# Performance work log

Measured on AMD Instinct MI355X. Metric: run time of the kernel, lower is better.

## Reference

```python
import jax, jax.numpy as jnp
import numpy as np

TAU = 0.2          # rank_temperature
LAM = 8.0          # lambda_value
TOPO = 0.5         # topology_influence
LEN_C = 0.01       # edge_length_coeff
SP_C = 0.001       # edge_sparsity_coeff
B, M, D = 4096, 256, 256


def _pairwise_sq(a, b):
    # [Na, D] x [Nb, D] -> [Na, Nb] squared L2 distances
    sq = (jnp.sum(a * a, -1)[:, None] - 2.0 * (a @ b.T)
          + jnp.sum(b * b, -1)[None, :])
    return jnp.maximum(sq, 0.0)


def setup_inputs() -> dict:
    key = jax.random.key(0)
    k1, k2, k3 = jax.random.split(key, 3)
    data = jax.random.normal(k1, (B, D), dtype=jnp.float32)
    weights = jax.random.uniform(k2, (M, D), dtype=jnp.float32)
    # edge logits initialized near edge_init_logit (-2.0) with small noise
    edge_logits = -2.0 + 0.1 * jax.random.normal(k3, (M, M), dtype=jnp.float32)
    return {"data": data, "weights": weights, "edge_logits": edge_logits}


def reference(data, weights, edge_logits):
    m = weights.shape[0]
    eye = jnp.eye(m, dtype=data.dtype)

    # distances: [B, M], l2
    distances = jnp.sqrt(_pairwise_sq(data, weights))

    # soft rank: [B, M]; pairwise sigmoid with zeroed diagonal
    diff = (distances[:, :, None] - distances[:, None, :]) / TAU  # [B, M, M]
    prob_greater = jax.nn.sigmoid(diff) * (1.0 - eye)[None]
    soft_rank = 1.0 + jnp.sum(prob_greater, axis=-1)

    # exponential neighborhood weighting
    neighborhood = jnp.exp(-(soft_rank - 1.0) / LAM)

    # symmetric edge probabilities with zero diagonal
    logits = 0.5 * (edge_logits + edge_logits.T)
    edge_prob = jax.nn.sigmoid(logits) * (1.0 - eye)

    degree = jnp.sum(edge_prob, axis=1) / float(m - 1)
    neighborhood = neighborhood * (1.0 + TOPO * degree[None, :])

    data_term = jnp.mean(neighborhood * distances)

    proto_dist = _pairwise_sq(weights, weights)  # sq_l2
    weighted_len = jnp.sum(edge_prob * proto_dist) / (jnp.sum(edge_prob) + 1e-8)
    sparsity = jnp.mean(edge_prob)

    loss = data_term + LEN_C * weighted_len + SP_C * sparsity
    return loss
```

## Files before the change

### kernel.cpp

```cpp
#include <hip/hip_runtime.h>
#include <math.h>

#define B_N 4096
#define M_N 256
#define D_N 256
#define ROWS 4
#define GRID_MAIN (B_N / ROWS)
#define NSLOT 64
#define BLK_PER_SLOT (GRID_MAIN / NSLOT)

constexpr float TAU_   = 0.2f;
constexpr float LAM_   = 8.0f;
constexpr float TOPO_  = 0.5f;
constexpr float LEN_C_ = 0.01f;
constexpr float SP_C_  = 0.001f;
constexpr float LOG2E_ = 1.44269504088896340736f;
constexpr float KSC    = LOG2E_ / TAU_;
constexpr float KL     = LOG2E_ / LAM_;
constexpr float C0_    = 133.0f;


__device__ __forceinline__ float wave_reduce_sum(float v) {
#pragma unroll
  for (int off = 1; off < 64; off <<= 1) v += __shfl_xor(v, off, 64);
  return v;
}

__device__ __forceinline__ void rank_quad(float iv, float iv2, float4 q,
                                          float& s) {
  float ta = fmaf(q.x, iv, 1.0f);
  float da = fmaf(q.y, iv2, ta);
  float na = ta + 1.0f;
  float tb = fmaf(q.z, iv, 1.0f);
  float db = fmaf(q.w, iv2, tb);
  float nb = tb + 1.0f;
  float d4 = da * db;
  float n4 = fmaf(na, db, nb * da);
  s = fmaf(n4, __builtin_amdgcn_rcpf(d4), s);
}

__global__ __launch_bounds__(256) void k_prep(const float* __restrict__ w,
                                              const float* __restrict__ E,
                                              float* __restrict__ ws) {
  int tid = threadIdx.x;
  if (blockIdx.x < M_N) {
    float* wT = ws + 8192;
    int j = blockIdx.x, d = tid;
    float v = w[j * D_N + d];
    wT[d * M_N + j] = v;
    float s = wave_reduce_sum(v * v);
    __shared__ float red[4];
    if ((d & 63) == 0) red[d >> 6] = s;
    if (j == 0) {
      if (d < 16) ws[d] = 0.0f;
      if (d < NSLOT) {
        ws[2048 + 16 * d] = 0.0f;
        ((unsigned*)ws)[4096 + 16 * d] = 0u;
      }
    }
    __syncthreads();
    if (d == 0) ws[512 + j] = red[0] + red[1] + red[2] + red[3];
  } else {
    int j = blockIdx.x - M_N;
    int k = tid;
    __shared__ __align__(16) float sp[M_N];
    __shared__ float redp[4], redt[4];

    float l = 0.5f * (E[j * M_N + k] + E[k * M_N + j]);
    float p = __builtin_amdgcn_rcpf(1.0f + __builtin_amdgcn_exp2f(-l * LOG2E_));
    if (k == j) p = 0.0f;
    sp[k] = p;

    float spw = wave_reduce_sum(p);
    if ((k & 63) == 0) redp[k >> 6] = spw;
    __syncthreads();
    float tp = redp[0] + redp[1] + redp[2] + redp[3];

    float A = 0.0f, Bv = 0.0f;
    const float4* sp4 = (const float4*)sp;
    const float* wb = w + tid;
#pragma unroll 4
    for (int k0 = 0; k0 < M_N / 4; k0++) {
      float4 pq = sp4[k0];
      const float* wr = wb + (size_t)(4 * k0) * D_N;
      float w0 = wr[0], w1 = wr[D_N], w2 = wr[2 * D_N], w3 = wr[3 * D_N];
      A  = fmaf(pq.x, w0 * w0, A); Bv = fmaf(pq.x, w0, Bv);
      A  = fmaf(pq.y, w1 * w1, A); Bv = fmaf(pq.y, w1, Bv);
      A  = fmaf(pq.z, w2 * w2, A); Bv = fmaf(pq.z, w2, Bv);
      A  = fmaf(pq.w, w3 * w3, A); Bv = fmaf(pq.w, w3, Bv);
    }

    float wj = w[j * D_N + tid];
    float v  = fmaf(tp, wj * wj, fmaf(-2.0f * wj, Bv, A));
    float sv = wave_reduce_sum(v);
    if ((k & 63) == 0) redt[k >> 6] = sv;
    __syncthreads();
    if (k == 0) {
      float tw = redt[0] + redt[1] + redt[2] + redt[3];
      ws[16 + j]   = tp * (1.0f / (float)(M_N - 1));
      ws[1024 + j] = tp;
      ws[1280 + j] = tw;
    }
  }
}

__global__ __launch_bounds__(256, 4) void k_main(const float* __restrict__ data,
                                                 float* __restrict__ ws,
                                                 float* __restrict__ out) {
  const float* wT     = ws + 8192;
  const float* wnorm  = ws + 512;
  const float* degree = ws + 16;
  float* S_slot  = ws + 2048;
  unsigned* cnt1 = (unsigned*)ws + 4096;
  unsigned* cnt2 = (unsigned*)ws + 4;

  __shared__ __align__(16) float ew[ROWS][M_N];
  __shared__ __align__(16) float ewp[ROWS][M_N];
  __shared__ float rednrm[ROWS][4];
  __shared__ float snrm[ROWS];
  __shared__ float redf[4], redp[4], redw[4];
  __shared__ int isLast;

  const int tid  = threadIdx.x;
  const int wv_  = tid >> 6;
  const int lane = tid & 63;
  const int b0   = blockIdx.x * ROWS;

#pragma unroll
  for (int r = 0; r < ROWS; r++) {
    float x = data[(size_t)(b0 + r) * D_N + tid];
    float s = wave_reduce_sum(x * x);
    if (lane == 0) rednrm[r][wv_] = s;
  }
  __syncthreads();
  if (tid < ROWS)
    snrm[tid] = rednrm[tid][0] + rednrm[tid][1] + rednrm[tid][2] + rednrm[tid][3];

  const float4* x0 = (const float4*)(data + (size_t)(b0 + 0) * D_N);
  const float4* x1 = (const float4*)(data + (size_t)(b0 + 1) * D_N);
  const float4* x2 = (const float4*)(data + (size_t)(b0 + 2) * D_N);
  const float4* x3 = (const float4*)(data + (size_t)(b0 + 3) * D_N);
  const float* pw = wT + tid;

  float a0 = 0.f, a1 = 0.f, a2 = 0.f, a3 = 0.f;
  float wreg[2][16];
#pragma unroll
  for (int i = 0; i < 16; i++) wreg[0][i] = pw[(size_t)i * M_N];

#pragma unroll
  for (int g = 0; g < 16; g++) {
    const int cur = g & 1, nxt = cur ^ 1;
    if (g < 15) {
#pragma unroll
      for (int i = 0; i < 16; i++)
        wreg[nxt][i] = pw[(size_t)((g + 1) * 16 + i) * M_N];
    }
#pragma unroll
    for (int i4 = 0; i4 < 4; i4++) {
      int d4 = 4 * g + i4;
      float4 xa = x0[d4], xb = x1[d4], xc = x2[d4], xd = x3[d4];
      float w0 = wreg[cur][4 * i4 + 0], w1 = wreg[cur][4 * i4 + 1];
      float w2 = wreg[cur][4 * i4 + 2], w3 = wreg[cur][4 * i4 + 3];
      a0 = fmaf(xa.x, w0, a0); a0 = fmaf(xa.y, w1, a0);
      a0 = fmaf(xa.z, w2, a0); a0 = fmaf(xa.w, w3, a0);
      a1 = fmaf(xb.x, w0, a1); a1 = fmaf(xb.y, w1, a1);
      a1 = fmaf(xb.z, w2, a1); a1 = fmaf(xb.w, w3, a1);
      a2 = fmaf(xc.x, w0, a2); a2 = fmaf(xc.y, w1, a2);
      a2 = fmaf(xc.z, w2, a2); a2 = fmaf(xc.w, w3, a2);
      a3 = fmaf(xd.x, w0, a3); a3 = fmaf(xd.y, w1, a3);
      a3 = fmaf(xd.z, w2, a3); a3 = fmaf(xd.w, w3, a3);
    }
  }
  __syncthreads();

  float wn = wnorm[tid];
  float acc[ROWS] = {a0, a1, a2, a3};
  float dist[ROWS], iv[ROWS], iv2[ROWS];
#pragma unroll
  for (int r = 0; r < ROWS; r++) {
    float sq = snrm[r] - 2.0f * acc[r] + wn;
    dist[r] = sqrtf(fmaxf(sq, 0.0f));
    float sc = dist[r] * KSC;
    ew[r][tid] = __builtin_amdgcn_exp2f(sc - C0_);
    iv[r]      = __builtin_amdgcn_exp2f(C0_ - sc);
    iv2[r]     = iv[r] * iv[r];
  }
  __syncthreads();

#pragma unroll
  for (int h = 0; h < 2; h++) {
    int p  = tid + h * 256;
    int r  = p >> 7, idx = p & 127;
    float ea = ew[r][2 * idx], eb = ew[r][2 * idx + 1];
    ewp[r][2 * idx]     = ea + eb;
    ewp[r][2 * idx + 1] = ea * eb;
  }
  __syncthreads();

  float fj = 1.0f + TOPO_ * degree[tid];
  float tl = 0.0f;
#pragma unroll
  for (int r = 0; r < ROWS; r++) {
    float s = 0.0f;
    const float4* q4 = (const float4*)(&ewp[r][0]);
    float ivr = iv[r], iv2r = iv2[r];
#pragma unroll 8
    for (int k4 = 0; k4 < M_N / 4; k4++) {
      float4 q = q4[k4];
      rank_quad(ivr, iv2r, q, s);
    }
    float nb = __builtin_amdgcn_exp2f((0.5f - s) * KL);
    tl = fmaf(nb * dist[r], fj, tl);
  }

  float bs = wave_reduce_sum(tl);
  if (lane == 0) redf[wv_] = bs;
  __syncthreads();
  if (tid == 0) {
    float tot = redf[0] + redf[1] + redf[2] + redf[3];
    int slot = (int)(blockIdx.x & (NSLOT - 1));
    float old = atomicAdd(&S_slot[16 * slot], tot);
    asm volatile("" : "+v"(old));
    int last = 0;
    unsigned t1 = atomicAdd(&cnt1[16 * slot], 1u);
    if (t1 == (unsigned)(BLK_PER_SLOT - 1)) {
      unsigned t2 = atomicAdd(cnt2, 1u);
      last = (t2 == (unsigned)(NSLOT - 1)) ? 1 : 0;
    }
    isLast = last;
  }
  __syncthreads();

  if (isLast) {
    float p  = ws[1024 + tid];
    float wd = ws[1280 + tid];
    float rp = wave_reduce_sum(p);
    float rw = wave_reduce_sum(wd);
    if (lane == 0) { redp[wv_] = rp; redw[wv_] = rw; }
    float sd = 0.0f;
    if (wv_ == 0) {
      float v = atomicAdd(&S_slot[16 * lane], 0.0f);
      sd = wave_reduce_sum(v);
    }
    __syncthreads();
    if (tid == 0) {
      float Sp   = redp[0] + redp[1] + redp[2] + redp[3];
      float Swpd = redw[0] + redw[1] + redw[2] + redw[3];
      float data_term = sd * (1.0f / ((float)B_N * (float)M_N));
      float wl = Swpd / (Sp + 1e-8f);
      float sparsity = Sp * (1.0f / ((float)M_N * (float)M_N));
      out[0] = data_term + LEN_C_ * wl + SP_C_ * sparsity;
    }
  }
}

extern "C" void kernel_launch(void* const* d_in, const int* in_sizes, int n_in,
                              void* d_out, int out_size, void* d_ws, size_t ws_size,
                              hipStream_t stream) {
  const float* data = (const float*)d_in[0];
  const float* w    = (const float*)d_in[1];
  const float* E    = (const float*)d_in[2];
  float* ws = (float*)d_ws;

  k_prep<<<2 * M_N, 256, 0, stream>>>(w, E, ws);
  k_main<<<GRID_MAIN, 256, 0, stream>>>(data, ws, (float*)d_out);
}
```

Baseline: 100.9 us.

## Compute data-prototype dot products with split-bf16 MFMA instead of scalar FMA

Replaces the per-thread FP32 FMA loop for the data·weights dot products with bf16 MFMA 16x16x32 instructions. Both operands are split into high and low bf16 parts and three products are accumulated to approximate FP32 accuracy. The prep kernel now stores the weights as row-major bf16 hi/lo arrays, and k_main stages the data rows as bf16 hi/lo in shared memory and writes the results through a new shared dotq buffer. With only 4 rows per block, most of each 16-row MFMA tile is wasted, since rows repeat across columns. The split-bf16 scheme also drops the lo*lo term, which adds a small precision loss.

```diff
diff --git a/kernel.cpp b/kernel.cpp
--- a/kernel.cpp
+++ b/kernel.cpp
@@ -20,10 +20,22 @@
 constexpr float C0_    = 133.0f;
 
 
+typedef __attribute__((ext_vector_type(8))) short bf16x8;
+typedef __attribute__((ext_vector_type(4))) float f32x4;
+
 __device__ __forceinline__ float wave_reduce_sum(float v) {
 #pragma unroll
   for (int off = 1; off < 64; off <<= 1) v += __shfl_xor(v, off, 64);
   return v;
+}
+
+__device__ __forceinline__ unsigned short f2bf(float f) {
+  unsigned u = __float_as_uint(f);
+  unsigned r = (u + 0x7FFFu + ((u >> 16) & 1u)) >> 16;
+  return (unsigned short)r;
+}
+__device__ __forceinline__ float bf2f(unsigned short h) {
+  return __uint_as_float(((unsigned)h) << 16);
 }
 
 __device__ __forceinline__ void rank_quad(float iv, float iv2, float4 q,
@@ -44,10 +56,15 @@
                                               float* __restrict__ ws) {
   int tid = threadIdx.x;
   if (blockIdx.x < M_N) {
-    float* wT = ws + 8192;
+    unsigned short* wbh = (unsigned short*)(ws + 8192);
+    unsigned short* wbl = (unsigned short*)(ws + 40960);
     int j = blockIdx.x, d = tid;
     float v = w[j * D_N + d];
-    wT[d * M_N + j] = v;
+    unsigned short h = f2bf(v);
+    float hf = bf2f(h);
+    unsigned short lo = f2bf(v - hf);
+    wbh[j * D_N + d] = h;
+    wbl[j * D_N + d] = lo;
     float s = wave_reduce_sum(v * v);
     __shared__ float red[4];
     if ((d & 63) == 0) red[d >> 6] = s;
@@ -107,7 +124,8 @@
 __global__ __launch_bounds__(256, 4) void k_main(const float* __restrict__ data,
                                                  float* __restrict__ ws,
                                                  float* __restrict__ out) {
-  const float* wT     = ws + 8192;
+  const unsigned short* wbh = (const unsigned short*)(ws + 8192);
+  const unsigned short* wbl = (const unsigned short*)(ws + 40960);
   const float* wnorm  = ws + 512;
   const float* degree = ws + 16;
   float* S_slot  = ws + 2048;
@@ -116,6 +134,8 @@
 
   __shared__ __align__(16) float ew[ROWS][M_N];
   __shared__ __align__(16) float ewp[ROWS][M_N];
+  __shared__ __align__(16) float dotq[M_N][4];
+  __shared__ __align__(16) unsigned short xh[ROWS][264], xl[ROWS][264];
   __shared__ float rednrm[ROWS][4];
   __shared__ float snrm[ROWS];
   __shared__ float redf[4], redp[4], redw[4];
@@ -131,54 +151,52 @@
     float x = data[(size_t)(b0 + r) * D_N + tid];
     float s = wave_reduce_sum(x * x);
     if (lane == 0) rednrm[r][wv_] = s;
+    unsigned short h = f2bf(x);
+    float hf = bf2f(h);
+    xh[r][tid] = h;
+    xl[r][tid] = f2bf(x - hf);
   }
   __syncthreads();
   if (tid < ROWS)
     snrm[tid] = rednrm[tid][0] + rednrm[tid][1] + rednrm[tid][2] + rednrm[tid][3];
 
-  const float4* x0 = (const float4*)(data + (size_t)(b0 + 0) * D_N);
-  const float4* x1 = (const float4*)(data + (size_t)(b0 + 1) * D_N);
-  const float4* x2 = (const float4*)(data + (size_t)(b0 + 2) * D_N);
-  const float4* x3 = (const float4*)(data + (size_t)(b0 + 3) * D_N);
-  const float* pw = wT + tid;
-
-  float a0 = 0.f, a1 = 0.f, a2 = 0.f, a3 = 0.f;
-  float wreg[2][16];
-#pragma unroll
-  for (int i = 0; i < 16; i++) wreg[0][i] = pw[(size_t)i * M_N];
-
-#pragma unroll
-  for (int g = 0; g < 16; g++) {
-    const int cur = g & 1, nxt = cur ^ 1;
-    if (g < 15) {
-#pragma unroll
-      for (int i = 0; i < 16; i++)
-        wreg[nxt][i] = pw[(size_t)((g + 1) * 16 + i) * M_N];
-    }
-#pragma unroll
-    for (int i4 = 0; i4 < 4; i4++) {
-      int d4 = 4 * g + i4;
-      float4 xa = x0[d4], xb = x1[d4], xc = x2[d4], xd = x3[d4];
-      float w0 = wreg[cur][4 * i4 + 0], w1 = wreg[cur][4 * i4 + 1];
-      float w2 = wreg[cur][4 * i4 + 2], w3 = wreg[cur][4 * i4 + 3];
-      a0 = fmaf(xa.x, w0, a0); a0 = fmaf(xa.y, w1, a0);
-      a0 = fmaf(xa.z, w2, a0); a0 = fmaf(xa.w, w3, a0);
-      a1 = fmaf(xb.x, w0, a1); a1 = fmaf(xb.y, w1, a1);
-      a1 = fmaf(xb.z, w2, a1); a1 = fmaf(xb.w, w3, a1);
-      a2 = fmaf(xc.x, w0, a2); a2 = fmaf(xc.y, w1, a2);
-      a2 = fmaf(xc.z, w2, a2); a2 = fmaf(xc.w, w3, a2);
-      a3 = fmaf(xd.x, w0, a3); a3 = fmaf(xd.y, w1, a3);
-      a3 = fmaf(xd.z, w2, a3); a3 = fmaf(xd.w, w3, a3);
+  {
+    const int colr = lane & 15;
+    const int kg   = lane >> 4;
+    const int r4   = colr & 3;
+
+    bf16x8 afh[8], afl[8];
+#pragma unroll
+    for (int k0 = 0; k0 < 8; k0++) {
+      afh[k0] = *(const bf16x8*)&xh[r4][k0 * 32 + kg * 8];
+      afl[k0] = *(const bf16x8*)&xl[r4][k0 * 32 + kg * 8];
+    }
+
+#pragma unroll
+    for (int t = 0; t < 4; t++) {
+      const int jt = (wv_ << 2) + t;
+      const unsigned short* bh = wbh + ((jt * 16 + colr) << 8) + (kg << 3);
+      const unsigned short* bl = wbl + ((jt * 16 + colr) << 8) + (kg << 3);
+      f32x4 acc = {0.0f, 0.0f, 0.0f, 0.0f};
+#pragma unroll
+      for (int k0 = 0; k0 < 8; k0++) {
+        bf16x8 bfh = *(const bf16x8*)(bh + (k0 << 5));
+        bf16x8 bfl = *(const bf16x8*)(bl + (k0 << 5));
+        acc = __builtin_amdgcn_mfma_f32_16x16x32_bf16(afh[k0], bfh, acc, 0, 0, 0);
+        acc = __builtin_amdgcn_mfma_f32_16x16x32_bf16(afh[k0], bfl, acc, 0, 0, 0);
+        acc = __builtin_amdgcn_mfma_f32_16x16x32_bf16(afl[k0], bfh, acc, 0, 0, 0);
+      }
+      if (lane < 16) *(f32x4*)&dotq[(jt << 4) + lane][0] = acc;
     }
   }
   __syncthreads();
 
   float wn = wnorm[tid];
-  float acc[ROWS] = {a0, a1, a2, a3};
+  f32x4 dq = *(const f32x4*)&dotq[tid][0];
   float dist[ROWS], iv[ROWS], iv2[ROWS];
 #pragma unroll
   for (int r = 0; r < ROWS; r++) {
-    float sq = snrm[r] - 2.0f * acc[r] + wn;
+    float sq = snrm[r] - 2.0f * dq[r] + wn;
     dist[r] = sqrtf(fmaxf(sq, 0.0f));
     float sc = dist[r] * KSC;
     ew[r][tid] = __builtin_amdgcn_exp2f(sc - C0_);
```

Result: slower. 119.8 us (+18.7%).
